# Performance work log

Hardware: AMD Instinct MI355X
Metric: run time of the kernel (lower is better)

## Reference

```python
import jax, jax.numpy as jnp
import numpy as np

NUM_SLOTS = 3
NUM_ORIENTS = 8
PATCH_SIZE = 81  # 9x9 board
BUY_SIZE = NUM_SLOTS * NUM_ORIENTS * PATCH_SIZE  # 1944
ACTIONS = 1 + PATCH_SIZE + BUY_SIZE  # 2026
NEG = -1.0e9
EPS = 1e-5

B = 4096
C_IN = 256
HID = 256


def setup_inputs() -> dict:
    key = jax.random.key(0)
    ks = jax.random.split(key, 12)
    s = 0.05
    return {
        "x": jax.random.normal(ks[0], (B, C_IN, 9, 9), jnp.float32),
        "action_mask": jax.random.randint(ks[1], (B, ACTIONS), 0, 2, dtype=jnp.int32),
        # p_conv: 1x1 conv, no bias (use_batch_norm=True) -> weight (HID, C_IN)
        "conv_w": jax.random.normal(ks[2], (HID, C_IN), jnp.float32) * s,
        # BatchNorm2d (inference form with running stats)
        "bn_gamma": jnp.ones((HID,), jnp.float32),
        "bn_beta": jnp.zeros((HID,), jnp.float32),
        "bn_mean": jax.random.normal(ks[3], (HID,), jnp.float32) * 0.1,
        "bn_var": jax.random.uniform(ks[4], (HID,), jnp.float32, 0.5, 1.5),
        "type_w": jax.random.normal(ks[5], (3, HID), jnp.float32) * s,
        "type_b": jnp.zeros((3,), jnp.float32),
        "patch_w": jax.random.normal(ks[6], (1, HID), jnp.float32) * s,
        "patch_b": jnp.zeros((1,), jnp.float32),
        "slot_w": jax.random.normal(ks[7], (NUM_SLOTS, HID), jnp.float32) * s,
        "slot_b": jnp.zeros((NUM_SLOTS,), jnp.float32),
        "orient_w": jax.random.normal(ks[8], (NUM_SLOTS * NUM_ORIENTS, HID), jnp.float32) * s,
        "orient_b": jnp.zeros((NUM_SLOTS * NUM_ORIENTS,), jnp.float32),
        "pos_w": jax.random.normal(ks[9], (NUM_SLOTS * NUM_ORIENTS, HID), jnp.float32) * s,
        "pos_b": jnp.zeros((NUM_SLOTS * NUM_ORIENTS,), jnp.float32),
    }


def _masked_logsoftmax(logits, mask_bool):
    lg = jnp.where(mask_bool, logits, NEG)
    return jnp.maximum(jax.nn.log_softmax(lg, axis=-1), -100.0)


def reference(x, action_mask, conv_w, bn_gamma, bn_beta, bn_mean, bn_var,
              type_w, type_b, patch_w, patch_b, slot_w, slot_b,
              orient_w, orient_b, pos_w, pos_b):
    b = x.shape[0]
    # 1x1 conv + BN (eval) + ReLU
    p = jnp.einsum('bchw,oc->bohw', x, conv_w)
    scale = bn_gamma * jax.lax.rsqrt(bn_var + EPS)
    p = jax.nn.relu(p * scale[None, :, None, None] + (bn_beta - bn_mean * scale)[None, :, None, None])
    p_mean = p.mean(axis=(2, 3))  # (B, HID)

    # masks from action_mask layout [pass | 81 patch | 1944 buy]
    am = action_mask > 0
    patch_mask = am[:, 1:1 + PATCH_SIZE]
    buy4d = am[:, 82:82 + BUY_SIZE].reshape(b, NUM_SLOTS, NUM_ORIENTS, PATCH_SIZE)
    type_mask = jnp.stack([am[:, 0], patch_mask.any(-1), buy4d.reshape(b, -1).any(-1)], axis=-1)
    orient_mask = buy4d.any(-1)
    slot_mask = orient_mask.any(-1)

    type_lp = _masked_logsoftmax(p_mean @ type_w.T + type_b, type_mask)          # (B,3)
    patch_logits = jnp.einsum('bchw,oc->bohw', p, patch_w).reshape(b, PATCH_SIZE) \
        + patch_b[0]
    patch_lp = _masked_logsoftmax(patch_logits, patch_mask)                       # (B,81)
    slot_lp = _masked_logsoftmax(p_mean @ slot_w.T + slot_b, slot_mask)           # (B,3)
    orient_lp = _masked_logsoftmax(
        (p_mean @ orient_w.T + orient_b).reshape(b, NUM_SLOTS, NUM_ORIENTS), orient_mask)
    pos_logits = (jnp.einsum('bchw,oc->bohw', p, pos_w) + pos_b[None, :, None, None]) \
        .reshape(b, NUM_SLOTS, NUM_ORIENTS, PATCH_SIZE)
    pos_lp = _masked_logsoftmax(pos_logits, buy4d)                                # (B,3,8,81)

    pass_lp = type_lp[:, 0:1]
    patch_joint = type_lp[:, 1:2] + patch_lp
    buy_joint = (type_lp[:, 2:3, None, None] + slot_lp[:, :, None, None]
                 + orient_lp[:, :, :, None] + pos_lp).reshape(b, BUY_SIZE)
    return jnp.concatenate([pass_lp, patch_joint, buy_joint], axis=1)  # (B, 2026)
```

## Files before the change

kernel.cpp:

```cpp
#include <hip/hip_runtime.h>

#define ACT 2026
#define NEGV -1.0e9f

typedef short short8 __attribute__((ext_vector_type(8)));
typedef float f32x4 __attribute__((ext_vector_type(4)));

__device__ __forceinline__ unsigned f2bf(float f) {
  unsigned u = __float_as_uint(f);
  return (u + 0x7FFFu + ((u >> 16) & 1u)) >> 16;
}

__device__ __forceinline__ unsigned cvtpk(float lo, float hi) {
  unsigned r;
  asm("v_cvt_pk_bf16_f32 %0, %1, %2" : "=v"(r) : "v"(lo), "v"(hi));
  return r;
}

#define GL16(gp, lp) __builtin_amdgcn_global_load_lds(                         \
    (const __attribute__((address_space(1))) void*)(gp),                       \
    (__attribute__((address_space(3))) void*)(lp), 16, 0, 0)

__global__ void prep_w_kernel(const float* __restrict__ conv_w,
                              const float* __restrict__ pos_w,
                              const float* __restrict__ patch_w,
                              unsigned short* __restrict__ wimg,
                              unsigned short* __restrict__ w2img) {
  int g = blockIdx.x * 256 + threadIdx.x;
  if (g < 8192) {
    int r = g & 15, gq = (g >> 4) & 3, mtg = (g >> 6) & 15, ks = g >> 10;
    const float* src = conv_w + (mtg * 16 + r) * 256 + ks * 32 + gq * 8;
    unsigned v0 = f2bf(src[0]) | (f2bf(src[1]) << 16);
    unsigned v1 = f2bf(src[2]) | (f2bf(src[3]) << 16);
    unsigned v2 = f2bf(src[4]) | (f2bf(src[5]) << 16);
    unsigned v3 = f2bf(src[6]) | (f2bf(src[7]) << 16);
    uint4 q; q.x = v0; q.y = v1; q.z = v2; q.w = v3;
    *(uint4*)(wimg + g * 8) = q;
  } else if (g < 9216) {
    int g2 = g - 8192;
    int r = g2 & 15, gq = (g2 >> 4) & 3, mt = (g2 >> 6) & 1, ks2 = g2 >> 7;
    int m2 = mt * 16 + r;
    int o0 = ks2 * 32 + gq * 8;
    unsigned short v[8];
#pragma unroll
    for (int e = 0; e < 8; ++e) {
      float f = 0.f;
      if (m2 < 24) f = pos_w[m2 * 256 + o0 + e];
      else if (m2 == 24) f = patch_w[o0 + e];
      v[e] = (unsigned short)f2bf(f);
    }
    uint4 q;
    q.x = (unsigned)v[0] | ((unsigned)v[1] << 16);
    q.y = (unsigned)v[2] | ((unsigned)v[3] << 16);
    q.z = (unsigned)v[4] | ((unsigned)v[5] << 16);
    q.w = (unsigned)v[6] | ((unsigned)v[7] << 16);
    *(uint4*)(w2img + g2 * 8) = q;
  }
}

__global__ __launch_bounds__(256, 3)
void policy_main(const float* __restrict__ x,
                 const int* __restrict__ am,
                 const unsigned short* __restrict__ wimg,
                 const unsigned short* __restrict__ w2img,
                 const float* __restrict__ bn_gamma, const float* __restrict__ bn_beta,
                 const float* __restrict__ bn_mean, const float* __restrict__ bn_var,
                 const float* __restrict__ type_w, const float* __restrict__ type_b,
                 const float* __restrict__ patch_b,
                 const float* __restrict__ slot_w, const float* __restrict__ slot_b,
                 const float* __restrict__ orient_w, const float* __restrict__ orient_b,
                 const float* __restrict__ pos_b,
                 float* __restrict__ out)
{
  __shared__ __align__(16) char s_big[49152];
  __shared__ __align__(16) float s_scale[256];
  __shared__ __align__(16) float s_bias[256];
  __shared__ __align__(16) float s_pmean[256];
  __shared__ float s_part[240];
  __shared__ float s_hl[30];
  __shared__ float s_tlp[3], s_slp[3], s_olp[24];
  __shared__ int s_omask[24];
  __shared__ int s_misc[6];

  char* f32buf = s_big;
  char* bfimg  = s_big + 20736;
  unsigned short* pT = (unsigned short*)s_big;
  float* s_out2 = (float*)s_big;

  const int tid = threadIdx.x;
  const int w  = tid >> 6;
  const int l  = tid & 63;
  const int b  = blockIdx.x;
  const float* xb = x + (size_t)b * (256 * 81);

  {
    float sc = bn_gamma[tid] * rsqrtf(bn_var[tid] + 1e-5f);
    s_scale[tid] = sc;
    s_bias[tid]  = bn_beta[tid] - bn_mean[tid] * sc;
  }

  const int kg = l >> 4;
  const int kr = l & 15;
  const int g4 = kg * 4;

  f32x4 acc[4][6];
#pragma unroll
  for (int i = 0; i < 4; ++i)
#pragma unroll
    for (int j = 0; j < 6; ++j) {
      f32x4 z = {0.f, 0.f, 0.f, 0.f};
      acc[i][j] = z;
    }

  auto STAGE = [&](int ks) {
    const char* g = (const char*)xb + ks * 10368;
    char* lb = f32buf + (ks & 1) * 10368;
    GL16(g + tid * 16,         lb + w * 1024);
    GL16(g + (256 + tid) * 16, lb + 4096 + w * 1024);
    if (tid < 136)   GL16(g + (512 + tid) * 16, lb + 8192 + w * 1024);
    else if (w == 3) GL16(g + (576 + l) * 16,   lb + 9216);
  };

  auto TRANSPOSE = [&](int t) {
    const float* src = (const float*)(f32buf + (t & 1) * 10368);
    char* dst = bfimg + (t & 1) * 6144;
    {
      int q = tid;
      int nt_ = q >> 6, kr_ = (q >> 2) & 15, kg_ = q & 3;
      const float* s = src + kg_ * 648 + nt_ * 16 + kr_;
      uint4 v;
      v.x = cvtpk(s[0],   s[81]);
      v.y = cvtpk(s[162], s[243]);
      v.z = cvtpk(s[324], s[405]);
      v.w = cvtpk(s[486], s[567]);
      *(uint4*)(dst + q * 16) = v;
    }
    if (tid < 128) {
      int q = 256 + tid;
      int nt_ = q >> 6, kr_ = (q >> 2) & 15, kg_ = q & 3;
      const float* s = src + kg_ * 648 + nt_ * 16 + kr_;
      uint4 v;
      v.x = cvtpk(s[0],   s[81]);
      v.y = cvtpk(s[162], s[243]);
      v.z = cvtpk(s[324], s[405]);
      v.w = cvtpk(s[486], s[567]);
      *(uint4*)(dst + q * 16) = v;
    }
  };

  STAGE(0);
  STAGE(1);
  __syncthreads();
  TRANSPOSE(0);
  __syncthreads();

  const int fragoff = (kr * 4 + kg) * 16;

  auto STEP = [&](int k) {
    if (k + 2 < 8) STAGE(k + 2);
    short8 af[4];
    {
      const unsigned short* ab = wimg + k * 8192 + w * 2048 + kg * 128 + kr * 8;
      af[0] = *(const short8*)(ab);
      af[1] = *(const short8*)(ab + 512);
      af[2] = *(const short8*)(ab + 1024);
      af[3] = *(const short8*)(ab + 1536);
    }
    if (k + 1 < 8) TRANSPOSE(k + 1);
    const char* bi = bfimg + (k & 1) * 6144;
#pragma unroll
    for (int nt = 0; nt < 6; ++nt) {
      short8 bf = *(const short8*)(bi + nt * 1024 + fragoff);
      acc[0][nt] = __builtin_amdgcn_mfma_f32_16x16x32_bf16(af[0], bf, acc[0][nt], 0, 0, 0);
      acc[1][nt] = __builtin_amdgcn_mfma_f32_16x16x32_bf16(af[1], bf, acc[1][nt], 0, 0, 0);
      acc[2][nt] = __builtin_amdgcn_mfma_f32_16x16x32_bf16(af[2], bf, acc[2][nt], 0, 0, 0);
      acc[3][nt] = __builtin_amdgcn_mfma_f32_16x16x32_bf16(af[3], bf, acc[3][nt], 0, 0, 0);
    }
    __syncthreads();
  };

  STEP(0); STEP(1); STEP(2); STEP(3);
  STEP(4); STEP(5); STEP(6); STEP(7);

#pragma unroll
  for (int mi = 0; mi < 4; ++mi) {
    int ob = w * 64 + mi * 16 + g4;
    float sc0 = s_scale[ob], sc1 = s_scale[ob + 1], sc2 = s_scale[ob + 2], sc3 = s_scale[ob + 3];
    float bi0 = s_bias[ob],  bi1 = s_bias[ob + 1],  bi2 = s_bias[ob + 2],  bi3 = s_bias[ob + 3];
    float vs0 = 0.f, vs1 = 0.f, vs2 = 0.f, vs3 = 0.f;
    int ks2 = ob >> 5;
    int j2  = (ob >> 3) & 3;
    int e0  = ob & 7;
    char* pbase = (char*)pT + ks2 * 6144 + j2 * 256 + kr * 16 + e0 * 2;
#pragma unroll
    for (int nt = 0; nt < 6; ++nt) {
      float v0 = fmaxf(acc[mi][nt][0] * sc0 + bi0, 0.f);
      float v1 = fmaxf(acc[mi][nt][1] * sc1 + bi1, 0.f);
      float v2 = fmaxf(acc[mi][nt][2] * sc2 + bi2, 0.f);
      float v3 = fmaxf(acc[mi][nt][3] * sc3 + bi3, 0.f);
      if (nt < 5 || kr == 0) { vs0 += v0; vs1 += v1; vs2 += v2; vs3 += v3; }
      uint2 pvv;
      pvv.x = cvtpk(v0, v1);
      pvv.y = cvtpk(v2, v3);
      *(uint2*)(pbase + nt * 1024) = pvv;
    }
    float vv[4] = {vs0, vs1, vs2, vs3};
#pragma unroll
    for (int i = 0; i < 4; ++i) {
      float s = vv[i];
      s += __shfl_xor(s, 1);
      s += __shfl_xor(s, 2);
      s += __shfl_xor(s, 4);
      s += __shfl_xor(s, 8);
      vv[i] = s;
    }
    if (kr == 0) {
      s_pmean[ob]     = vv[0] * (1.f / 81.f);
      s_pmean[ob + 1] = vv[1] * (1.f / 81.f);
      s_pmean[ob + 2] = vv[2] * (1.f / 81.f);
      s_pmean[ob + 3] = vv[3] * (1.f / 81.f);
    }
  }

  const int* amr = am + (size_t)b * ACT;
  for (int t = w; t < 25; t += 4) {
    int off = (t < 24) ? (82 + t * 81) : 1;
    int v1 = amr[off + l];
    int v2 = (l < 17) ? amr[off + 64 + l] : 0;
    unsigned long long bal = __ballot((v1 | v2) != 0);
    if (l == 0) {
      int any = (bal != 0ULL) ? 1 : 0;
      if (t < 24) s_omask[t] = any; else s_misc[0] = any;
    }
  }
  __syncthreads();

  {
    const int mt  = w & 1;
    const int ntb = (w >> 1) * 3;
    f32x4 acc2[3];
#pragma unroll
    for (int t = 0; t < 3; ++t) { f32x4 z = {0.f, 0.f, 0.f, 0.f}; acc2[t] = z; }
#pragma unroll
    for (int ks2 = 0; ks2 < 8; ++ks2) {
      const unsigned short* ap = w2img + ((ks2 * 2 + mt) * 4 + kg) * 128 + kr * 8;
      short8 a2 = *(const short8*)ap;
#pragma unroll
      for (int t = 0; t < 3; ++t) {
        const short8* bp = (const short8*)((const char*)pT + ks2 * 6144 + (ntb + t) * 1024 + kg * 256 + kr * 16);
        acc2[t] = __builtin_amdgcn_mfma_f32_16x16x32_bf16(a2, *bp, acc2[t], 0, 0, 0);
      }
    }
    __syncthreads();
#pragma unroll
    for (int t = 0; t < 3; ++t) {
      int hw = (ntb + t) * 16 + kr;
      int m2 = mt * 16 + g4;
#pragma unroll
      for (int i = 0; i < 4; ++i)
        s_out2[(m2 + i) * 104 + hw] = acc2[t][i];
    }
  }

  if (tid < 240) {
    int h = tid >> 3, seg = tid & 7;
    const float* wp = (h < 3) ? (type_w + h * 256)
                    : (h < 6) ? (slot_w + (h - 3) * 256)
                              : (orient_w + (h - 6) * 256);
    float p = 0.f;
    int base = seg * 32;
#pragma unroll 8
    for (int e = 0; e < 32; ++e) p += s_pmean[base + e] * wp[base + e];
    s_part[tid] = p;
  }
  __syncthreads();

  if (tid < 30) {
    float a = 0.f;
#pragma unroll
    for (int e = 0; e < 8; ++e) a += s_part[tid * 8 + e];
    a += (tid < 3) ? type_b[tid] : (tid < 6) ? slot_b[tid - 3] : orient_b[tid - 6];
    s_hl[tid] = a;
  }
  if (tid == 32) {
    int sa0 = 0, sa1 = 0, sa2 = 0;
#pragma unroll
    for (int r = 0; r < 8; ++r) { sa0 |= s_omask[r]; sa1 |= s_omask[8 + r]; sa2 |= s_omask[16 + r]; }
    s_misc[1] = sa0; s_misc[2] = sa1; s_misc[3] = sa2;
    s_misc[4] = sa0 | sa1 | sa2;
  }
  __syncthreads();

  if (tid == 0) {
    int mk0 = amr[0] > 0, mk1 = s_misc[0], mk2 = s_misc[4];
    float g0 = mk0 ? s_hl[0] : NEGV;
    float g1 = mk1 ? s_hl[1] : NEGV;
    float g2 = mk2 ? s_hl[2] : NEGV;
    float m = fmaxf(fmaxf(g0, g1), g2);
    float sum = __expf(g0 - m) + __expf(g1 - m) + __expf(g2 - m);
    float ls = m + __logf(sum);
    s_tlp[0] = fmaxf(g0 - ls, -100.f);
    s_tlp[1] = fmaxf(g1 - ls, -100.f);
    s_tlp[2] = fmaxf(g2 - ls, -100.f);
  } else if (tid == 1) {
    float g[3]; float m = -3.0e38f;
#pragma unroll
    for (int s = 0; s < 3; ++s) { g[s] = s_misc[1 + s] ? s_hl[3 + s] : NEGV; m = fmaxf(m, g[s]); }
    float sum = 0.f;
#pragma unroll
    for (int s = 0; s < 3; ++s) sum += __expf(g[s] - m);
    float ls = m + __logf(sum);
#pragma unroll
    for (int s = 0; s < 3; ++s) s_slp[s] = fmaxf(g[s] - ls, -100.f);
  } else if (tid >= 2 && tid < 5) {
    int s = tid - 2;
    float g[8]; float m = -3.0e38f;
#pragma unroll
    for (int r = 0; r < 8; ++r) { g[r] = s_omask[s * 8 + r] ? s_hl[6 + s * 8 + r] : NEGV; m = fmaxf(m, g[r]); }
    float sum = 0.f;
#pragma unroll
    for (int r = 0; r < 8; ++r) sum += __expf(g[r] - m);
    float ls = m + __logf(sum);
#pragma unroll
    for (int r = 0; r < 8; ++r) s_olp[s * 8 + r] = fmaxf(g[r] - ls, -100.f);
  }
  __syncthreads();

  float* ob_out = out + (size_t)b * ACT;
  for (int t = w; t < 25; t += 4) {
    int off = (t < 24) ? (82 + t * 81) : 1;
    float badd = (t < 24) ? pos_b[t] : patch_b[0];
    int a1 = amr[off + l];
    int a2v = (l < 17) ? amr[off + 64 + l] : 0;
    float lg1 = (a1 > 0) ? (s_out2[t * 104 + l] + badd) : NEGV;
    float lg2 = (l < 17 && a2v > 0) ? (s_out2[t * 104 + 64 + l] + badd) : NEGV;
    float mx = fmaxf(lg1, (l < 17) ? lg2 : -3.0e38f);
#pragma unroll
    for (int mm = 1; mm < 64; mm <<= 1) mx = fmaxf(mx, __shfl_xor(mx, mm));
    float sm = __expf(lg1 - mx) + ((l < 17) ? __expf(lg2 - mx) : 0.f);
#pragma unroll
    for (int mm = 1; mm < 64; mm <<= 1) sm += __shfl_xor(sm, mm);
    float lse = mx + __logf(sm);
    float lp1 = fmaxf(lg1 - lse, -100.f);
    float lp2 = fmaxf(lg2 - lse, -100.f);
    float addj; int obase;
    if (t < 24) { addj = s_tlp[2] + s_slp[t >> 3] + s_olp[t]; obase = 82 + t * 81; }
    else        { addj = s_tlp[1];                             obase = 1; }
    ob_out[obase + l] = addj + lp1;
    if (l < 17) ob_out[obase + 64 + l] = addj + lp2;
    if (t == 24 && l == 0) ob_out[0] = s_tlp[0];
  }
}

extern "C" void kernel_launch(void* const* d_in, const int* in_sizes, int n_in,
                              void* d_out, int out_size, void* d_ws, size_t ws_size,
                              hipStream_t stream) {
  (void)in_sizes; (void)n_in; (void)out_size; (void)ws_size;
  const float* x        = (const float*)d_in[0];
  const int*   amask    = (const int*)d_in[1];
  const float* conv_w   = (const float*)d_in[2];
  const float* bn_gamma = (const float*)d_in[3];
  const float* bn_beta  = (const float*)d_in[4];
  const float* bn_mean  = (const float*)d_in[5];
  const float* bn_var   = (const float*)d_in[6];
  const float* type_w   = (const float*)d_in[7];
  const float* type_b   = (const float*)d_in[8];
  const float* patch_w  = (const float*)d_in[9];
  const float* patch_b  = (const float*)d_in[10];
  const float* slot_w   = (const float*)d_in[11];
  const float* slot_b   = (const float*)d_in[12];
  const float* orient_w = (const float*)d_in[13];
  const float* orient_b = (const float*)d_in[14];
  const float* pos_w    = (const float*)d_in[15];
  const float* pos_b    = (const float*)d_in[16];
  float* outp = (float*)d_out;

  unsigned short* wimg  = (unsigned short*)d_ws;
  unsigned short* w2img = wimg + 65536;

  prep_w_kernel<<<36, 256, 0, stream>>>(conv_w, pos_w, patch_w, wimg, w2img);
  policy_main<<<4096, 256, 0, stream>>>(x, amask, wimg, w2img,
                                        bn_gamma, bn_beta, bn_mean, bn_var,
                                        type_w, type_b, patch_b,
                                        slot_w, slot_b, orient_w, orient_b,
                                        pos_b, outp);
}
```

Measured before the change: 216.6 us.

## Triple-buffer global-to-LDS staging with explicit vmcnt waits instead of syncthreads

Expands the fp32 staging area from two to three LDS buffers so that global loads for step k+3 are issued while step k computes. The full __syncthreads is replaced by s_waitcnt vmcnt/lgkmcnt plus s_barrier, so each step waits only for the oldest outstanding loads. Each wave now issues exactly three uniform 16-byte loads, which keeps the vmcnt counts consistent. The cost is more LDS use, since the bf16 image moves to offset 31104, and the pipeline now depends on hand-counted vmcnt values and sched_barriers being correct.

Measured after the change: 200.0 us. 1.08x faster.

```diff
diff --git a/kernel.cpp b/kernel.cpp
--- a/kernel.cpp
+++ b/kernel.cpp
@@ -83,7 +83,7 @@
   __shared__ int s_misc[6];
 
   char* f32buf = s_big;
-  char* bfimg  = s_big + 20736;
+  char* bfimg  = s_big + 31104;
   unsigned short* pT = (unsigned short*)s_big;
   float* s_out2 = (float*)s_big;
 
@@ -114,15 +114,17 @@
 
   auto STAGE = [&](int ks) {
     const char* g = (const char*)xb + ks * 10368;
-    char* lb = f32buf + (ks & 1) * 10368;
-    GL16(g + tid * 16,         lb + w * 1024);
-    GL16(g + (256 + tid) * 16, lb + 4096 + w * 1024);
-    if (tid < 136)   GL16(g + (512 + tid) * 16, lb + 8192 + w * 1024);
-    else if (w == 3) GL16(g + (576 + l) * 16,   lb + 9216);
+    char* lb = f32buf + (ks % 3) * 10368;
+    int o1 = w * 162;
+    int o2 = o1 + 64;
+    int o3 = (w == 3) ? 584 : o1 + 128;
+    GL16(g + (o1 + l) * 16, lb + o1 * 16);
+    GL16(g + (o2 + l) * 16, lb + o2 * 16);
+    GL16(g + (o3 + l) * 16, lb + o3 * 16);
   };
 
   auto TRANSPOSE = [&](int t) {
-    const float* src = (const float*)(f32buf + (t & 1) * 10368);
+    const float* src = (const float*)(f32buf + (t % 3) * 10368);
     char* dst = bfimg + (t & 1) * 6144;
     {
       int q = tid;
@@ -148,16 +150,19 @@
     }
   };
 
-  STAGE(0);
-  STAGE(1);
-  __syncthreads();
+  STAGE(0); STAGE(1); STAGE(2);
+  asm volatile("s_waitcnt vmcnt(6)" ::: "memory");
+  __builtin_amdgcn_s_barrier();
+  __builtin_amdgcn_sched_barrier(0);
   TRANSPOSE(0);
-  __syncthreads();
+  asm volatile("s_waitcnt vmcnt(3)" ::: "memory");
+  asm volatile("s_waitcnt lgkmcnt(0)" ::: "memory");
+  __builtin_amdgcn_s_barrier();
+  __builtin_amdgcn_sched_barrier(0);
 
   const int fragoff = (kr * 4 + kg) * 16;
 
   auto STEP = [&](int k) {
-    if (k + 2 < 8) STAGE(k + 2);
     short8 af[4];
     {
       const unsigned short* ab = wimg + k * 8192 + w * 2048 + kg * 128 + kr * 8;
@@ -166,6 +171,8 @@
       af[2] = *(const short8*)(ab + 1024);
       af[3] = *(const short8*)(ab + 1536);
     }
+    __builtin_amdgcn_sched_barrier(0);
+    if (k + 3 < 8) STAGE(k + 3);
     if (k + 1 < 8) TRANSPOSE(k + 1);
     const char* bi = bfimg + (k & 1) * 6144;
 #pragma unroll
@@ -176,7 +183,15 @@
       acc[2][nt] = __builtin_amdgcn_mfma_f32_16x16x32_bf16(af[2], bf, acc[2][nt], 0, 0, 0);
       acc[3][nt] = __builtin_amdgcn_mfma_f32_16x16x32_bf16(af[3], bf, acc[3][nt], 0, 0, 0);
     }
-    __syncthreads();
+    if (k < 7) {
+      if (k + 3 < 8) asm volatile("s_waitcnt vmcnt(3)" ::: "memory");
+      else           asm volatile("s_waitcnt vmcnt(0)" ::: "memory");
+      asm volatile("s_waitcnt lgkmcnt(0)" ::: "memory");
+      __builtin_amdgcn_s_barrier();
+      __builtin_amdgcn_sched_barrier(0);
+    } else {
+      __syncthreads();
+    }
   };
 
   STEP(0); STEP(1); STEP(2); STEP(3);
```
